# Optimization experiments

Measured on AMD Instinct MI355X. Metric: run time of the kernel, lower is better.

## Reference

```python
import jax, jax.numpy as jnp
import numpy as np

H = 32
W = 32
HIDDEN = 64
NUM_CLASSES = 10
BATCH = 128


def setup_inputs() -> dict:
    key = jax.random.key(0)
    ks = jax.random.split(key, 5)
    D = 4 * HIDDEN * H * W  # number_of_output_dimensions()
    return {
        "x": jax.random.normal(ks[0], (BATCH, 1, H, W), jnp.float32),
        "w_in": jax.random.normal(ks[1], (HIDDEN, 1), jnp.float32) * 0.1,
        "b_in": jnp.zeros((HIDDEN,), jnp.float32),
        "w_state": jax.random.normal(ks[2], (HIDDEN, HIDDEN, 2), jnp.float32) * (1.0 / np.sqrt(2 * HIDDEN)),
        "b_state": jnp.zeros((HIDDEN,), jnp.float32),
        "w_fc": jax.random.normal(ks[3], (D, NUM_CLASSES), jnp.float32) * 0.01,
        "b_fc": jnp.zeros((NUM_CLASSES,), jnp.float32),
    }


def _skew(x):
    # x: [B,1,H,W] -> [B,1,H,W+H-1]; row r shifted right by r (diagonal skew)
    Ws = W + H - 1
    col = jnp.arange(Ws)[None, :] - jnp.arange(H)[:, None]  # [H,Ws]
    valid = ((col >= 0) & (col < W)).astype(x.dtype)
    colc = jnp.clip(col, 0, W - 1)
    rows = jnp.arange(H)[:, None]
    return x[:, :, rows, colc] * valid[None, None]


def _one_direction(x, w_in, b_in, w_state, b_state):
    # Diagonal-scan MDRNN over skewed columns.
    B = x.shape[0]
    xs = _skew(x)  # [B,1,H,Ws]
    # Input projection for all columns at once (1x1 conv equivalent)
    xin = jnp.einsum('oc,bchw->bohw', w_in, xs) + b_in[None, :, None, None]
    cols = jnp.moveaxis(xin, 3, 0)  # [Ws,B,HIDDEN,H]

    w_up, w_same = w_state[:, :, 0], w_state[:, :, 1]

    def step(h, xc):
        # conv1d(kernel=2, padding=1) over column, bottom padding removed:
        # out[r] = w_up @ h[r-1] + w_same @ h[r]
        h_up = jnp.pad(h, ((0, 0), (0, 0), (1, 0)))[:, :, :H]
        s = (jnp.einsum('oi,bir->bor', w_up, h_up)
             + jnp.einsum('oi,bir->bor', w_same, h)
             + b_state[None, :, None])
        hn = jnp.tanh(s + xc)
        return hn, hn

    h0 = jnp.zeros((B, HIDDEN, H), x.dtype)
    _, ys = jax.lax.scan(step, h0, cols)  # [Ws,B,HIDDEN,H]
    acts = jnp.moveaxis(ys, 0, 3)  # [B,HIDDEN,H,Ws]
    # Unskew: out[..., r, c] = acts[..., r, c + r]
    ccols = jnp.arange(W)[None, :] + jnp.arange(H)[:, None]  # [H,W]
    rows = jnp.arange(H)[:, None]
    return acts[:, :, rows, ccols]  # [B,HIDDEN,H,W]


def reference(x, w_in, b_in, w_state, b_state, w_fc, b_fc):
    B = x.shape[0]
    # Four scanning directions via flips on dims 2 and 3, concatenated on batch
    x2 = x[:, :, ::-1, :]
    x3 = x[:, :, :, ::-1]
    x4 = x[:, :, ::-1, ::-1]
    xm = jnp.concatenate([x, x2, x3, x4], axis=0)  # [4B,1,H,W]
    acts = _one_direction(xm, w_in, b_in, w_state, b_state)  # [4B,HIDDEN,H,W]
    # index_select interleaving: example b gets its 4 direction copies contiguously
    sel = (jnp.arange(B)[:, None] + B * jnp.arange(4)[None, :]).reshape(-1)
    a = acts[sel].reshape(B, -1)  # [B, 4*HIDDEN*H*W]
    logits = a @ w_fc + b_fc
    return jax.nn.log_softmax(logits, axis=-1)
```

## Files before the change

kernel.cpp:

```cpp
#include <hip/hip_runtime.h>
#include <hip/hip_bf16.h>

#define NHID 64
#define NT   63
#define NBD  512
#define HLDS_STR 72
#define XSTR 35

typedef __attribute__((ext_vector_type(8))) short bf16x8;
typedef __attribute__((ext_vector_type(4))) float f32x4;

__device__ __forceinline__ float tanh_fast(float x) {
    const float e = __expf(2.0f * x);
    const float r = __builtin_amdgcn_rcpf(e + 1.0f);
    return 1.0f - 2.0f * r;
}

__device__ __forceinline__ unsigned int cvt_pk_bf16(float lo, float hi) {
    unsigned int r;
    asm("v_cvt_pk_bf16_f32 %0, %1, %2" : "=v"(r) : "v"(lo), "v"(hi));
    return r;
}

__device__ __forceinline__ float bf2f(unsigned int u16) {
    return __uint_as_float(u16 << 16);
}

#define SKEW_R0(t)  ((t) > 31 ? (t) - 31 : 0)
#define SKEW_R1(t)  ((t) < 31 ? (t) : 31)
#define SKEW_OFF(t) ((t) < 32 ? ((t) * ((t) + 1)) >> 1 : 1024 - (((63 - (t)) * (64 - (t))) >> 1))

#define LGKM_BARRIER() do {                                   \
    asm volatile("s_waitcnt lgkmcnt(0)" ::: "memory");        \
    __builtin_amdgcn_s_barrier();                             \
    asm volatile("" ::: "memory");                            \
} while (0)

__global__ __launch_bounds__(256, 4) void k_main(
    const float* __restrict__ x,
    const float* __restrict__ w_in,
    const float* __restrict__ b_in,
    const float* __restrict__ w_state,
    const float* __restrict__ b_state,
    unsigned short* __restrict__ acts_c,
    const float* __restrict__ w_fc,
    unsigned short* __restrict__ wt_swz)
{
    __shared__ __align__(16) unsigned short h0buf[33 * HLDS_STR];
    __shared__ __align__(16) unsigned short h1buf[33 * HLDS_STR];
    __shared__ float xs[32 * XSTR];

    const int tid = threadIdx.x;

    if (blockIdx.x >= 512) {
        const int rel = blockIdx.x - 512;
        const int t   = rel >> 6;
        const int sub = rel & 63;
        const int r0 = SKEW_R0(t), r1 = SKEW_R1(t);
        const int cnt = r1 - r0 + 1;
        const int span = cnt << 10;
        int f = sub * 2048 + tid * 8;
        const int fdst = f;
        if (f >= 4 * span) return;
        int d = 0;
        while (f >= span) { f -= span; ++d; }
        const int ks   = f >> 9;
        const int lane = (f >> 3) & 63;
        const int g = lane >> 4, n = lane & 15;
        unsigned int pk[4];
        #pragma unroll
        for (int jj = 0; jj < 4; ++jj) {
            float v[2] = {0.0f, 0.0f};
            #pragma unroll
            for (int h = 0; h < 2; ++h) {
                const int j = jj * 2 + h;
                const int k = ks * 32 + g * 8 + j;
                const int r = r0 + (k >> 6);
                const int o = k & 63;
                const int c = t - r;
                if (n < 10)
                    v[h] = w_fc[((((size_t)(d * 64 + o)) << 10) + (r << 5) + c) * 10 + n];
            }
            pk[jj] = cvt_pk_bf16(v[0], v[1]);
        }
        uint4 st; st.x = pk[0]; st.y = pk[1]; st.z = pk[2]; st.w = pk[3];
        *(uint4*)(wt_swz + (size_t)SKEW_OFF(t) * 4096 + fdst) = st;
        return;
    }

    const int bd  = blockIdx.x;
    const int d   = bd >> 7;
    const int b   = bd & 127;
    const int lane = tid & 63;
    const int wave = tid >> 6;
    const int wp = wave & 1;
    const int nt = wave >> 1;
    const int n  = lane & 15;
    const int g  = lane >> 4;

    const bool flr = (d & 1) != 0;
    const bool flc = (d & 2) != 0;
    const float* xb = x + (size_t)b * 1024;
    for (int idx = tid; idx < 1024; idx += 256) {
        const int r = idx >> 5, c = idx & 31;
        xs[r * XSTR + c] = xb[(flr ? 31 - r : r) * 32 + (flc ? 31 - c : c)];
    }

    for (int m2 = tid; m2 < (33 * HLDS_STR) / 2; m2 += 256) {
        ((unsigned int*)h0buf)[m2] = 0u;
        ((unsigned int*)h1buf)[m2] = 0u;
    }

    bf16x8 a0[4], a1[4];
    #pragma unroll
    for (int wl = 0; wl < 2; ++wl) {
        const int o = wp * 32 + wl * 16 + n;
        #pragma unroll
        for (int kt = 0; kt < 4; ++kt) {
            const int s  = kt >> 1;
            const int cb = (kt & 1) * 32 + g * 8;
            bf16x8 w8;
            #pragma unroll
            for (int j = 0; j < 8; ++j) {
                const float w = w_state[((size_t)o * 64 + cb + j) * 2 + s];
                w8[j] = (short)(cvt_pk_bf16(w, 0.0f) & 0xffffu);
            }
            if (wl == 0) a0[kt] = w8; else a1[kt] = w8;
        }
    }

    float biasr[2][4], winr[2][4];
    #pragma unroll
    for (int wl = 0; wl < 2; ++wl)
        #pragma unroll
        for (int j = 0; j < 4; ++j) {
            const int o = wp * 32 + wl * 16 + g * 4 + j;
            biasr[wl][j] = b_in[o] + b_state[o];
            winr[wl][j]  = w_in[o];
        }

    const int r_out = nt * 16 + n;
    const int rdoff = r_out * HLDS_STR + g * 8;
    const int wroff = (r_out + 1) * HLDS_STR;
    const int cb0 = wp * 32 + g * 4;
    const int tlo = nt * 16;
    const float* xs_r = &xs[r_out * XSTR];

    unsigned short* actp = acts_c + (size_t)bd * 65536 + (size_t)r_out * 1984 + cb0;

    __syncthreads();

#define STEP(T, RB, WB) do {                                                    \
    if ((unsigned)((T) - tlo) < 48u) {                                          \
        const bf16x8 b0 = *(const bf16x8*)&RB[rdoff];                           \
        const bf16x8 b1 = *(const bf16x8*)&RB[rdoff + 32];                      \
        const bf16x8 b2 = *(const bf16x8*)&RB[rdoff + HLDS_STR];                \
        const bf16x8 b3 = *(const bf16x8*)&RB[rdoff + HLDS_STR + 32];           \
        f32x4 s0a = {0,0,0,0}, s0b = {0,0,0,0};                                 \
        f32x4 s1a = {0,0,0,0}, s1b = {0,0,0,0};                                 \
        s0a = __builtin_amdgcn_mfma_f32_16x16x32_bf16(a0[0], b0, s0a, 0,0,0);   \
        s1a = __builtin_amdgcn_mfma_f32_16x16x32_bf16(a1[0], b0, s1a, 0,0,0);   \
        s0b = __builtin_amdgcn_mfma_f32_16x16x32_bf16(a0[2], b2, s0b, 0,0,0);   \
        s1b = __builtin_amdgcn_mfma_f32_16x16x32_bf16(a1[2], b2, s1b, 0,0,0);   \
        s0a = __builtin_amdgcn_mfma_f32_16x16x32_bf16(a0[1], b1, s0a, 0,0,0);   \
        s1a = __builtin_amdgcn_mfma_f32_16x16x32_bf16(a1[1], b1, s1a, 0,0,0);   \
        s0b = __builtin_amdgcn_mfma_f32_16x16x32_bf16(a0[3], b3, s0b, 0,0,0);   \
        s1b = __builtin_amdgcn_mfma_f32_16x16x32_bf16(a1[3], b3, s1b, 0,0,0);   \
        const int c_ = (T) - r_out;                                             \
        const float xv = ((unsigned)c_ < 32u) ? xs_r[c_ & 31] : 0.0f;           \
        uint2 pk0, pk1;                                                         \
        {                                                                       \
            const float h0 = tanh_fast(s0a[0] + s0b[0] + biasr[0][0] + winr[0][0] * xv); \
            const float h1 = tanh_fast(s0a[1] + s0b[1] + biasr[0][1] + winr[0][1] * xv); \
            const float h2 = tanh_fast(s0a[2] + s0b[2] + biasr[0][2] + winr[0][2] * xv); \
            const float h3 = tanh_fast(s0a[3] + s0b[3] + biasr[0][3] + winr[0][3] * xv); \
            pk0.x = cvt_pk_bf16(h0, h1); pk0.y = cvt_pk_bf16(h2, h3);           \
            *(uint2*)&WB[wroff + cb0] = pk0;                                    \
        }                                                                       \
        {                                                                       \
            const float h0 = tanh_fast(s1a[0] + s1b[0] + biasr[1][0] + winr[1][0] * xv); \
            const float h1 = tanh_fast(s1a[1] + s1b[1] + biasr[1][1] + winr[1][1] * xv); \
            const float h2 = tanh_fast(s1a[2] + s1b[2] + biasr[1][2] + winr[1][2] * xv); \
            const float h3 = tanh_fast(s1a[3] + s1b[3] + biasr[1][3] + winr[1][3] * xv); \
            pk1.x = cvt_pk_bf16(h0, h1); pk1.y = cvt_pk_bf16(h2, h3);           \
            *(uint2*)&WB[wroff + cb0 + 16] = pk1;                               \
        }                                                                       \
        if ((unsigned)c_ < 32u) {                                               \
            *(uint2*)(actp)      = pk0;                                         \
            *(uint2*)(actp + 16) = pk1;                                         \
        }                                                                       \
    }                                                                           \
    LGKM_BARRIER();                                                             \
    actp += 64;                                                                 \
} while (0)

    for (int sp = 0; sp < 31; ++sp) {
        const int t = 2 * sp;
        STEP(t,     h0buf, h1buf);
        STEP(t + 1, h1buf, h0buf);
    }
    STEP(62, h0buf, h1buf);
#undef STEP
}

__global__ __launch_bounds__(256, 4) void k_fc(
    const unsigned short* __restrict__ acts_c,
    const unsigned short* __restrict__ wt_swz,
    float* __restrict__ partial)
{
    const int tid = threadIdx.x;
    const int blk = blockIdx.x;
    const int t   = blk >> 3;
    const int d   = (blk >> 1) & 3;
    const int mh  = blk & 1;
    const int lane = tid & 63;
    const int wv  = tid >> 6;
    const int g   = lane >> 4;
    const int n   = lane & 15;

    const int r0 = SKEW_R0(t), r1 = SKEW_R1(t);
    const int cnt = r1 - r0 + 1;
    const int off = SKEW_OFF(t);

    const int tb = d * 128 + mh * 64 + wv * 16;
    const unsigned short* Ap = acts_c + (size_t)(tb + n) * 65536
                             + (size_t)r0 * 1984 + (size_t)t * 64 + g * 8;
    const unsigned short* Bp = wt_swz
        + ((size_t)off * 4 + (size_t)d * cnt) * 1024 + lane * 8;

    f32x4 acc = {0.f, 0.f, 0.f, 0.f};
    #pragma unroll 2
    for (int q = 0; q < cnt; ++q) {
        const bf16x8 a0  = *(const bf16x8*)(Ap);
        const bf16x8 bb0 = *(const bf16x8*)(Bp);
        const bf16x8 a1  = *(const bf16x8*)(Ap + 32);
        const bf16x8 bb1 = *(const bf16x8*)(Bp + 512);
        acc = __builtin_amdgcn_mfma_f32_16x16x32_bf16(a0, bb0, acc, 0, 0, 0);
        acc = __builtin_amdgcn_mfma_f32_16x16x32_bf16(a1, bb1, acc, 0, 0, 0);
        Ap += 1984;
        Bp += 1024;
    }
    const int batch = tb + g * 4;
    #pragma unroll
    for (int reg = 0; reg < 4; ++reg)
        partial[((size_t)t * 512 + batch + reg) * 16 + n] = acc[reg];
}

__global__ __launch_bounds__(256) void k_out(
    const float* __restrict__ partial,
    const float* __restrict__ b_fc,
    float* __restrict__ out)
{
    __shared__ float lred[252 * 10];
    __shared__ float lgs[10];
    __shared__ float lse;
    const int b = blockIdx.x;
    const int tid = threadIdx.x;
    if (tid < 252) {
        const int t = tid >> 2, d = tid & 3;
        const float* p = partial + ((size_t)t * 512 + d * 128 + b) * 16;
        #pragma unroll
        for (int n2 = 0; n2 < 10; ++n2) lred[tid * 10 + n2] = p[n2];
    }
    __syncthreads();
    if (tid < 10) {
        float s = b_fc[tid];
        for (int i = 0; i < 252; ++i) s += lred[i * 10 + tid];
        lgs[tid] = s;
    }
    __syncthreads();
    if (tid == 0) {
        float m = lgs[0];
        for (int nn = 1; nn < 10; ++nn) m = fmaxf(m, lgs[nn]);
        float ssum = 0.0f;
        for (int nn = 0; nn < 10; ++nn) ssum += __expf(lgs[nn] - m);
        lse = m + __logf(ssum);
    }
    __syncthreads();
    if (tid < 10) out[b * 10 + tid] = lgs[tid] - lse;
}

extern "C" void kernel_launch(void* const* d_in, const int* in_sizes, int n_in,
                              void* d_out, int out_size, void* d_ws, size_t ws_size,
                              hipStream_t stream)
{
    const float* x       = (const float*)d_in[0];
    const float* w_in    = (const float*)d_in[1];
    const float* b_in    = (const float*)d_in[2];
    const float* w_state = (const float*)d_in[3];
    const float* b_state = (const float*)d_in[4];
    const float* w_fc    = (const float*)d_in[5];
    const float* b_fc    = (const float*)d_in[6];
    float* out = (float*)d_out;

    unsigned short* wt_swz = (unsigned short*)d_ws;
    float* partial = (float*)((char*)d_ws + (size_t)(8u << 20));
    unsigned short* acts_c = (unsigned short*)((char*)d_ws + (size_t)(16u << 20));

    k_main<<<4544, 256, 0, stream>>>(x, w_in, b_in, w_state, b_state,
                                     acts_c, w_fc, wt_swz);
    k_fc  <<<504, 256, 0, stream>>>(acts_c, wt_swz, partial);
    k_out <<<128, 256, 0, stream>>>(partial, b_fc, out);
}
```

Baseline: 62.83 us.

## Replace block barriers with inter-wave LDS flags using two-wave recurrence blocks

The recurrence blocks shrink from four waves to two. Each wave now owns 16 rows and computes all 64 hidden outputs with 16 MFMAs per step. The per-step workgroup barrier is replaced by point-to-point LDS flags, where each wave spins with s_sleep until the partner wave has finished the previous step. The weight-prep blocks now process two chunks per thread to match the smaller block size. This aims to cut barrier cost, but doubles the serial MFMA and epilogue work per wave each step and adds spin-wait latency.

```diff
diff --git a/kernel.cpp b/kernel.cpp
--- a/kernel.cpp
+++ b/kernel.cpp
@@ -30,13 +30,38 @@
 #define SKEW_R1(t)  ((t) < 31 ? (t) : 31)
 #define SKEW_OFF(t) ((t) < 32 ? ((t) * ((t) + 1)) >> 1 : 1024 - (((63 - (t)) * (64 - (t))) >> 1))
 
-#define LGKM_BARRIER() do {                                   \
-    asm volatile("s_waitcnt lgkmcnt(0)" ::: "memory");        \
-    __builtin_amdgcn_s_barrier();                             \
-    asm volatile("" ::: "memory");                            \
-} while (0)
-
-__global__ __launch_bounds__(256, 4) void k_main(
+__device__ __forceinline__ void prep_one(
+    const float* __restrict__ w_fc, unsigned short* __restrict__ wt_swz,
+    int t, int r0, int span, int f)
+{
+    if (f >= 4 * span) return;
+    const int fdst = f;
+    int d = 0;
+    while (f >= span) { f -= span; ++d; }
+    const int ks   = f >> 9;
+    const int lane = (f >> 3) & 63;
+    const int g = lane >> 4, n = lane & 15;
+    unsigned int pk[4];
+    #pragma unroll
+    for (int jj = 0; jj < 4; ++jj) {
+        float v[2] = {0.0f, 0.0f};
+        #pragma unroll
+        for (int h = 0; h < 2; ++h) {
+            const int j = jj * 2 + h;
+            const int k = ks * 32 + g * 8 + j;
+            const int r = r0 + (k >> 6);
+            const int o = k & 63;
+            const int c = t - r;
+            if (n < 10)
+                v[h] = w_fc[((((size_t)(d * 64 + o)) << 10) + (r << 5) + c) * 10 + n];
+        }
+        pk[jj] = cvt_pk_bf16(v[0], v[1]);
+    }
+    uint4 st; st.x = pk[0]; st.y = pk[1]; st.z = pk[2]; st.w = pk[3];
+    *(uint4*)(wt_swz + (size_t)SKEW_OFF(t) * 4096 + fdst) = st;
+}
+
+__global__ __launch_bounds__(128, 2) void k_main(
     const float* __restrict__ x,
     const float* __restrict__ w_in,
     const float* __restrict__ b_in,
@@ -49,6 +74,7 @@
     __shared__ __align__(16) unsigned short h0buf[33 * HLDS_STR];
     __shared__ __align__(16) unsigned short h1buf[33 * HLDS_STR];
     __shared__ float xs[32 * XSTR];
+    __shared__ int sflags[2];
 
     const int tid = threadIdx.x;
 
@@ -57,34 +83,10 @@
         const int t   = rel >> 6;
         const int sub = rel & 63;
         const int r0 = SKEW_R0(t), r1 = SKEW_R1(t);
-        const int cnt = r1 - r0 + 1;
-        const int span = cnt << 10;
-        int f = sub * 2048 + tid * 8;
-        const int fdst = f;
-        if (f >= 4 * span) return;
-        int d = 0;
-        while (f >= span) { f -= span; ++d; }
-        const int ks   = f >> 9;
-        const int lane = (f >> 3) & 63;
-        const int g = lane >> 4, n = lane & 15;
-        unsigned int pk[4];
-        #pragma unroll
-        for (int jj = 0; jj < 4; ++jj) {
-            float v[2] = {0.0f, 0.0f};
-            #pragma unroll
-            for (int h = 0; h < 2; ++h) {
-                const int j = jj * 2 + h;
-                const int k = ks * 32 + g * 8 + j;
-                const int r = r0 + (k >> 6);
-                const int o = k & 63;
-                const int c = t - r;
-                if (n < 10)
-                    v[h] = w_fc[((((size_t)(d * 64 + o)) << 10) + (r << 5) + c) * 10 + n];
-            }
-            pk[jj] = cvt_pk_bf16(v[0], v[1]);
-        }
-        uint4 st; st.x = pk[0]; st.y = pk[1]; st.z = pk[2]; st.w = pk[3];
-        *(uint4*)(wt_swz + (size_t)SKEW_OFF(t) * 4096 + fdst) = st;
+        const int span = (r1 - r0 + 1) << 10;
+        const int f1 = sub * 2048 + tid * 8;
+        prep_one(w_fc, wt_swz, t, r0, span, f1);
+        prep_one(w_fc, wt_swz, t, r0, span, f1 + 1024);
         return;
     }
 
@@ -93,28 +95,27 @@
     const int b   = bd & 127;
     const int lane = tid & 63;
     const int wave = tid >> 6;
-    const int wp = wave & 1;
-    const int nt = wave >> 1;
     const int n  = lane & 15;
     const int g  = lane >> 4;
 
     const bool flr = (d & 1) != 0;
     const bool flc = (d & 2) != 0;
     const float* xb = x + (size_t)b * 1024;
-    for (int idx = tid; idx < 1024; idx += 256) {
+    for (int idx = tid; idx < 1024; idx += 128) {
         const int r = idx >> 5, c = idx & 31;
         xs[r * XSTR + c] = xb[(flr ? 31 - r : r) * 32 + (flc ? 31 - c : c)];
     }
 
-    for (int m2 = tid; m2 < (33 * HLDS_STR) / 2; m2 += 256) {
+    for (int m2 = tid; m2 < (33 * HLDS_STR) / 2; m2 += 128) {
         ((unsigned int*)h0buf)[m2] = 0u;
         ((unsigned int*)h1buf)[m2] = 0u;
     }
-
-    bf16x8 a0[4], a1[4];
+    if (tid == 0) { sflags[0] = 0; sflags[1] = 0; }
+
+    bf16x8 a[4][4];
     #pragma unroll
-    for (int wl = 0; wl < 2; ++wl) {
-        const int o = wp * 32 + wl * 16 + n;
+    for (int mt = 0; mt < 4; ++mt) {
+        const int o = mt * 16 + n;
         #pragma unroll
         for (int kt = 0; kt < 4; ++kt) {
             const int s  = kt >> 1;
@@ -125,73 +126,69 @@
                 const float w = w_state[((size_t)o * 64 + cb + j) * 2 + s];
                 w8[j] = (short)(cvt_pk_bf16(w, 0.0f) & 0xffffu);
             }
-            if (wl == 0) a0[kt] = w8; else a1[kt] = w8;
+            a[mt][kt] = w8;
         }
     }
 
-    float biasr[2][4], winr[2][4];
+    float biasr[4][4], winr[4][4];
     #pragma unroll
-    for (int wl = 0; wl < 2; ++wl)
+    for (int mt = 0; mt < 4; ++mt)
         #pragma unroll
         for (int j = 0; j < 4; ++j) {
-            const int o = wp * 32 + wl * 16 + g * 4 + j;
-            biasr[wl][j] = b_in[o] + b_state[o];
-            winr[wl][j]  = w_in[o];
+            const int o = mt * 16 + g * 4 + j;
+            biasr[mt][j] = b_in[o] + b_state[o];
+            winr[mt][j]  = w_in[o];
         }
 
-    const int r_out = nt * 16 + n;
+    const int r_out = wave * 16 + n;
     const int rdoff = r_out * HLDS_STR + g * 8;
-    const int wroff = (r_out + 1) * HLDS_STR;
-    const int cb0 = wp * 32 + g * 4;
-    const int tlo = nt * 16;
+    const int wroff = (r_out + 1) * HLDS_STR + g * 4;
+    const int tlo = wave * 16;
     const float* xs_r = &xs[r_out * XSTR];
-
-    unsigned short* actp = acts_c + (size_t)bd * 65536 + (size_t)r_out * 1984 + cb0;
+    volatile int* my_flag = (volatile int*)&sflags[wave];
+    volatile int* ot_flag = (volatile int*)&sflags[wave ^ 1];
+
+    unsigned short* actp = acts_c + (size_t)bd * 65536 + (size_t)r_out * 1984 + g * 4;
 
     __syncthreads();
 
-#define STEP(T, RB, WB) do {                                                    \
-    if ((unsigned)((T) - tlo) < 48u) {                                          \
-        const bf16x8 b0 = *(const bf16x8*)&RB[rdoff];                           \
-        const bf16x8 b1 = *(const bf16x8*)&RB[rdoff + 32];                      \
-        const bf16x8 b2 = *(const bf16x8*)&RB[rdoff + HLDS_STR];                \
-        const bf16x8 b3 = *(const bf16x8*)&RB[rdoff + HLDS_STR + 32];           \
-        f32x4 s0a = {0,0,0,0}, s0b = {0,0,0,0};                                 \
-        f32x4 s1a = {0,0,0,0}, s1b = {0,0,0,0};                                 \
-        s0a = __builtin_amdgcn_mfma_f32_16x16x32_bf16(a0[0], b0, s0a, 0,0,0);   \
-        s1a = __builtin_amdgcn_mfma_f32_16x16x32_bf16(a1[0], b0, s1a, 0,0,0);   \
-        s0b = __builtin_amdgcn_mfma_f32_16x16x32_bf16(a0[2], b2, s0b, 0,0,0);   \
-        s1b = __builtin_amdgcn_mfma_f32_16x16x32_bf16(a1[2], b2, s1b, 0,0,0);   \
-        s0a = __builtin_amdgcn_mfma_f32_16x16x32_bf16(a0[1], b1, s0a, 0,0,0);   \
-        s1a = __builtin_amdgcn_mfma_f32_16x16x32_bf16(a1[1], b1, s1a, 0,0,0);   \
-        s0b = __builtin_amdgcn_mfma_f32_16x16x32_bf16(a0[3], b3, s0b, 0,0,0);   \
-        s1b = __builtin_amdgcn_mfma_f32_16x16x32_bf16(a1[3], b3, s1b, 0,0,0);   \
-        const int c_ = (T) - r_out;                                             \
-        const float xv = ((unsigned)c_ < 32u) ? xs_r[c_ & 31] : 0.0f;           \
-        uint2 pk0, pk1;                                                         \
-        {                                                                       \
-            const float h0 = tanh_fast(s0a[0] + s0b[0] + biasr[0][0] + winr[0][0] * xv); \
-            const float h1 = tanh_fast(s0a[1] + s0b[1] + biasr[0][1] + winr[0][1] * xv); \
-            const float h2 = tanh_fast(s0a[2] + s0b[2] + biasr[0][2] + winr[0][2] * xv); \
-            const float h3 = tanh_fast(s0a[3] + s0b[3] + biasr[0][3] + winr[0][3] * xv); \
-            pk0.x = cvt_pk_bf16(h0, h1); pk0.y = cvt_pk_bf16(h2, h3);           \
-            *(uint2*)&WB[wroff + cb0] = pk0;                                    \
-        }                                                                       \
-        {                                                                       \
-            const float h0 = tanh_fast(s1a[0] + s1b[0] + biasr[1][0] + winr[1][0] * xv); \
-            const float h1 = tanh_fast(s1a[1] + s1b[1] + biasr[1][1] + winr[1][1] * xv); \
-            const float h2 = tanh_fast(s1a[2] + s1b[2] + biasr[1][2] + winr[1][2] * xv); \
-            const float h3 = tanh_fast(s1a[3] + s1b[3] + biasr[1][3] + winr[1][3] * xv); \
-            pk1.x = cvt_pk_bf16(h0, h1); pk1.y = cvt_pk_bf16(h2, h3);           \
-            *(uint2*)&WB[wroff + cb0 + 16] = pk1;                               \
-        }                                                                       \
-        if ((unsigned)c_ < 32u) {                                               \
-            *(uint2*)(actp)      = pk0;                                         \
-            *(uint2*)(actp + 16) = pk1;                                         \
-        }                                                                       \
-    }                                                                           \
-    LGKM_BARRIER();                                                             \
-    actp += 64;                                                                 \
+#define MFMA(F, B, C) C = __builtin_amdgcn_mfma_f32_16x16x32_bf16(F, B, C, 0, 0, 0)
+#define EPI(MT, AA, BB, WBUF) {                                                  \
+    const float h0 = tanh_fast(AA[0] + BB[0] + biasr[MT][0] + winr[MT][0] * xv); \
+    const float h1 = tanh_fast(AA[1] + BB[1] + biasr[MT][1] + winr[MT][1] * xv); \
+    const float h2 = tanh_fast(AA[2] + BB[2] + biasr[MT][2] + winr[MT][2] * xv); \
+    const float h3 = tanh_fast(AA[3] + BB[3] + biasr[MT][3] + winr[MT][3] * xv); \
+    uint2 pk; pk.x = cvt_pk_bf16(h0, h1); pk.y = cvt_pk_bf16(h2, h3);            \
+    *(uint2*)&WBUF[wroff + (MT) * 16] = pk;                                      \
+    if (stv) *(uint2*)(actp + (MT) * 16) = pk;                                   \
+}
+
+#define STEP(T, RB, WB) do {                                                     \
+    if ((unsigned)((T) - tlo) < 48u) {                                           \
+        while (*ot_flag < (T)) __builtin_amdgcn_s_sleep(1);                      \
+        const bf16x8 b0 = *(const bf16x8*)&RB[rdoff];                            \
+        const bf16x8 b1 = *(const bf16x8*)&RB[rdoff + 32];                       \
+        const bf16x8 b2 = *(const bf16x8*)&RB[rdoff + HLDS_STR];                 \
+        const bf16x8 b3 = *(const bf16x8*)&RB[rdoff + HLDS_STR + 32];            \
+        f32x4 A0 = {0,0,0,0}, A1 = {0,0,0,0}, A2 = {0,0,0,0}, A3 = {0,0,0,0};    \
+        f32x4 B0 = {0,0,0,0}, B1 = {0,0,0,0}, B2 = {0,0,0,0}, B3 = {0,0,0,0};    \
+        MFMA(a[0][0], b0, A0); MFMA(a[1][0], b0, A1);                            \
+        MFMA(a[2][0], b0, A2); MFMA(a[3][0], b0, A3);                            \
+        MFMA(a[0][2], b2, B0); MFMA(a[1][2], b2, B1);                            \
+        MFMA(a[2][2], b2, B2); MFMA(a[3][2], b2, B3);                            \
+        MFMA(a[0][1], b1, A0); MFMA(a[1][1], b1, A1);                            \
+        MFMA(a[2][1], b1, A2); MFMA(a[3][1], b1, A3);                            \
+        MFMA(a[0][3], b3, B0); MFMA(a[1][3], b3, B1);                            \
+        MFMA(a[2][3], b3, B2); MFMA(a[3][3], b3, B3);                            \
+        const int c_ = (T) - r_out;                                              \
+        const bool stv = (unsigned)c_ < 32u;                                     \
+        const float xv = stv ? xs_r[c_ & 31] : 0.0f;                             \
+        EPI(0, A0, B0, WB); EPI(1, A1, B1, WB);                                  \
+        EPI(2, A2, B2, WB); EPI(3, A3, B3, WB);                                  \
+        asm volatile("s_waitcnt lgkmcnt(0)" ::: "memory");                       \
+    }                                                                            \
+    if (lane == 0) *my_flag = (T) + 1;                                           \
+    actp += 64;                                                                  \
 } while (0)
 
     for (int sp = 0; sp < 31; ++sp) {
@@ -201,6 +198,8 @@
     }
     STEP(62, h0buf, h1buf);
 #undef STEP
+#undef EPI
+#undef MFMA
 }
 
 __global__ __launch_bounds__(256, 4) void k_fc(
@@ -297,7 +296,7 @@
     float* partial = (float*)((char*)d_ws + (size_t)(8u << 20));
     unsigned short* acts_c = (unsigned short*)((char*)d_ws + (size_t)(16u << 20));
 
-    k_main<<<4544, 256, 0, stream>>>(x, w_in, b_in, w_state, b_state,
+    k_main<<<4544, 128, 0, stream>>>(x, w_in, b_in, w_state, b_state,
                                      acts_c, w_fc, wt_swz);
     k_fc  <<<504, 256, 0, stream>>>(acts_c, wt_swz, partial);
     k_out <<<128, 256, 0, stream>>>(partial, b_fc, out);
```

Result: slower. 95.86 us (+52.6%).

## Process two batch sequences per block in recurrent scan kernel

Applied to the files above, without the earlier changes.

Each recurrent block now carries two independent (direction, batch) sequences through the diagonal scan, so the MFMA state-weight fragments are reused and the per-step barrier is shared by two sequences. This halves the number of scan blocks and doubles the independent MFMA work between barriers, which should hide latency in the serial 63-step chain. The cost is twice the shared memory per block, more registers, and a launch bound lowered to 2 blocks per SM. Total parallelism also drops to 256 scan blocks.

```diff
diff --git a/kernel.cpp b/kernel.cpp
--- a/kernel.cpp
+++ b/kernel.cpp
@@ -36,7 +36,7 @@
     asm volatile("" ::: "memory");                            \
 } while (0)
 
-__global__ __launch_bounds__(256, 4) void k_main(
+__global__ __launch_bounds__(256, 2) void k_main(
     const float* __restrict__ x,
     const float* __restrict__ w_in,
     const float* __restrict__ b_in,
@@ -46,14 +46,17 @@
     const float* __restrict__ w_fc,
     unsigned short* __restrict__ wt_swz)
 {
-    __shared__ __align__(16) unsigned short h0buf[33 * HLDS_STR];
-    __shared__ __align__(16) unsigned short h1buf[33 * HLDS_STR];
-    __shared__ float xs[32 * XSTR];
+    __shared__ __align__(16) unsigned short hA0[33 * HLDS_STR];
+    __shared__ __align__(16) unsigned short hA1[33 * HLDS_STR];
+    __shared__ __align__(16) unsigned short hB0[33 * HLDS_STR];
+    __shared__ __align__(16) unsigned short hB1[33 * HLDS_STR];
+    __shared__ float xsA[32 * XSTR];
+    __shared__ float xsB[32 * XSTR];
 
     const int tid = threadIdx.x;
 
-    if (blockIdx.x >= 512) {
-        const int rel = blockIdx.x - 512;
+    if (blockIdx.x >= 256) {
+        const int rel = blockIdx.x - 256;
         const int t   = rel >> 6;
         const int sub = rel & 63;
         const int r0 = SKEW_R0(t), r1 = SKEW_R1(t);
@@ -88,9 +91,11 @@
         return;
     }
 
-    const int bd  = blockIdx.x;
-    const int d   = bd >> 7;
-    const int b   = bd & 127;
+    const int blk = blockIdx.x;
+    const int bdA = 2 * blk;
+    const int bdB = 2 * blk + 1;
+    const int d   = bdA >> 7;
+    const int bA  = bdA & 127;
     const int lane = tid & 63;
     const int wave = tid >> 6;
     const int wp = wave & 1;
@@ -100,15 +105,19 @@
 
     const bool flr = (d & 1) != 0;
     const bool flc = (d & 2) != 0;
-    const float* xb = x + (size_t)b * 1024;
+    const float* xbA = x + (size_t)bA * 1024;
     for (int idx = tid; idx < 1024; idx += 256) {
         const int r = idx >> 5, c = idx & 31;
-        xs[r * XSTR + c] = xb[(flr ? 31 - r : r) * 32 + (flc ? 31 - c : c)];
+        const int src = (flr ? 31 - r : r) * 32 + (flc ? 31 - c : c);
+        xsA[r * XSTR + c] = xbA[src];
+        xsB[r * XSTR + c] = xbA[1024 + src];
     }
 
     for (int m2 = tid; m2 < (33 * HLDS_STR) / 2; m2 += 256) {
-        ((unsigned int*)h0buf)[m2] = 0u;
-        ((unsigned int*)h1buf)[m2] = 0u;
+        ((unsigned int*)hA0)[m2] = 0u;
+        ((unsigned int*)hA1)[m2] = 0u;
+        ((unsigned int*)hB0)[m2] = 0u;
+        ((unsigned int*)hB1)[m2] = 0u;
     }
 
     bf16x8 a0[4], a1[4];
@@ -144,63 +153,67 @@
     const int wroff = (r_out + 1) * HLDS_STR;
     const int cb0 = wp * 32 + g * 4;
     const int tlo = nt * 16;
-    const float* xs_r = &xs[r_out * XSTR];
-
-    unsigned short* actp = acts_c + (size_t)bd * 65536 + (size_t)r_out * 1984 + cb0;
+    const float* xsA_r = &xsA[r_out * XSTR];
+    const float* xsB_r = &xsB[r_out * XSTR];
+
+    unsigned short* actpA = acts_c + (size_t)bdA * 65536 + (size_t)r_out * 1984 + cb0;
+    unsigned short* actpB = acts_c + (size_t)bdB * 65536 + (size_t)r_out * 1984 + cb0;
 
     __syncthreads();
 
-#define STEP(T, RB, WB) do {                                                    \
-    if ((unsigned)((T) - tlo) < 48u) {                                          \
-        const bf16x8 b0 = *(const bf16x8*)&RB[rdoff];                           \
-        const bf16x8 b1 = *(const bf16x8*)&RB[rdoff + 32];                      \
-        const bf16x8 b2 = *(const bf16x8*)&RB[rdoff + HLDS_STR];                \
-        const bf16x8 b3 = *(const bf16x8*)&RB[rdoff + HLDS_STR + 32];           \
-        f32x4 s0a = {0,0,0,0}, s0b = {0,0,0,0};                                 \
-        f32x4 s1a = {0,0,0,0}, s1b = {0,0,0,0};                                 \
-        s0a = __builtin_amdgcn_mfma_f32_16x16x32_bf16(a0[0], b0, s0a, 0,0,0);   \
-        s1a = __builtin_amdgcn_mfma_f32_16x16x32_bf16(a1[0], b0, s1a, 0,0,0);   \
-        s0b = __builtin_amdgcn_mfma_f32_16x16x32_bf16(a0[2], b2, s0b, 0,0,0);   \
-        s1b = __builtin_amdgcn_mfma_f32_16x16x32_bf16(a1[2], b2, s1b, 0,0,0);   \
-        s0a = __builtin_amdgcn_mfma_f32_16x16x32_bf16(a0[1], b1, s0a, 0,0,0);   \
-        s1a = __builtin_amdgcn_mfma_f32_16x16x32_bf16(a1[1], b1, s1a, 0,0,0);   \
-        s0b = __builtin_amdgcn_mfma_f32_16x16x32_bf16(a0[3], b3, s0b, 0,0,0);   \
-        s1b = __builtin_amdgcn_mfma_f32_16x16x32_bf16(a1[3], b3, s1b, 0,0,0);   \
-        const int c_ = (T) - r_out;                                             \
-        const float xv = ((unsigned)c_ < 32u) ? xs_r[c_ & 31] : 0.0f;           \
-        uint2 pk0, pk1;                                                         \
-        {                                                                       \
-            const float h0 = tanh_fast(s0a[0] + s0b[0] + biasr[0][0] + winr[0][0] * xv); \
-            const float h1 = tanh_fast(s0a[1] + s0b[1] + biasr[0][1] + winr[0][1] * xv); \
-            const float h2 = tanh_fast(s0a[2] + s0b[2] + biasr[0][2] + winr[0][2] * xv); \
-            const float h3 = tanh_fast(s0a[3] + s0b[3] + biasr[0][3] + winr[0][3] * xv); \
-            pk0.x = cvt_pk_bf16(h0, h1); pk0.y = cvt_pk_bf16(h2, h3);           \
-            *(uint2*)&WB[wroff + cb0] = pk0;                                    \
-        }                                                                       \
-        {                                                                       \
-            const float h0 = tanh_fast(s1a[0] + s1b[0] + biasr[1][0] + winr[1][0] * xv); \
-            const float h1 = tanh_fast(s1a[1] + s1b[1] + biasr[1][1] + winr[1][1] * xv); \
-            const float h2 = tanh_fast(s1a[2] + s1b[2] + biasr[1][2] + winr[1][2] * xv); \
-            const float h3 = tanh_fast(s1a[3] + s1b[3] + biasr[1][3] + winr[1][3] * xv); \
-            pk1.x = cvt_pk_bf16(h0, h1); pk1.y = cvt_pk_bf16(h2, h3);           \
-            *(uint2*)&WB[wroff + cb0 + 16] = pk1;                               \
-        }                                                                       \
-        if ((unsigned)c_ < 32u) {                                               \
-            *(uint2*)(actp)      = pk0;                                         \
-            *(uint2*)(actp + 16) = pk1;                                         \
-        }                                                                       \
-    }                                                                           \
-    LGKM_BARRIER();                                                             \
-    actp += 64;                                                                 \
+#define MFMA(F, B, C) C = __builtin_amdgcn_mfma_f32_16x16x32_bf16(F, B, C, 0, 0, 0)
+#define EPI(WL, SA, SB, XV, WBUF, ACTP) {                                        \
+    const float h0 = tanh_fast(SA[0] + SB[0] + biasr[WL][0] + winr[WL][0] * (XV)); \
+    const float h1 = tanh_fast(SA[1] + SB[1] + biasr[WL][1] + winr[WL][1] * (XV)); \
+    const float h2 = tanh_fast(SA[2] + SB[2] + biasr[WL][2] + winr[WL][2] * (XV)); \
+    const float h3 = tanh_fast(SA[3] + SB[3] + biasr[WL][3] + winr[WL][3] * (XV)); \
+    uint2 pk; pk.x = cvt_pk_bf16(h0, h1); pk.y = cvt_pk_bf16(h2, h3);            \
+    *(uint2*)&WBUF[wroff + cb0 + (WL) * 16] = pk;                                \
+    if (stv) *(uint2*)((ACTP) + (WL) * 16) = pk;                                 \
+}
+
+#define STEP(T, RA_, WA_, RB_, WB_) do {                                         \
+    if ((unsigned)((T) - tlo) < 48u) {                                           \
+        const bf16x8 fA0 = *(const bf16x8*)&RA_[rdoff];                          \
+        const bf16x8 fA1 = *(const bf16x8*)&RA_[rdoff + 32];                     \
+        const bf16x8 fA2 = *(const bf16x8*)&RA_[rdoff + HLDS_STR];               \
+        const bf16x8 fA3 = *(const bf16x8*)&RA_[rdoff + HLDS_STR + 32];          \
+        const bf16x8 fB0 = *(const bf16x8*)&RB_[rdoff];                          \
+        const bf16x8 fB1 = *(const bf16x8*)&RB_[rdoff + 32];                     \
+        const bf16x8 fB2 = *(const bf16x8*)&RB_[rdoff + HLDS_STR];               \
+        const bf16x8 fB3 = *(const bf16x8*)&RB_[rdoff + HLDS_STR + 32];          \
+        f32x4 sA0a = {0,0,0,0}, sA0b = {0,0,0,0};                                \
+        f32x4 sA1a = {0,0,0,0}, sA1b = {0,0,0,0};                                \
+        f32x4 sB0a = {0,0,0,0}, sB0b = {0,0,0,0};                                \
+        f32x4 sB1a = {0,0,0,0}, sB1b = {0,0,0,0};                                \
+        MFMA(a0[0], fA0, sA0a); MFMA(a1[0], fA0, sA1a);                          \
+        MFMA(a0[0], fB0, sB0a); MFMA(a1[0], fB0, sB1a);                          \
+        MFMA(a0[2], fA2, sA0b); MFMA(a1[2], fA2, sA1b);                          \
+        MFMA(a0[2], fB2, sB0b); MFMA(a1[2], fB2, sB1b);                          \
+        MFMA(a0[1], fA1, sA0a); MFMA(a1[1], fA1, sA1a);                          \
+        MFMA(a0[1], fB1, sB0a); MFMA(a1[1], fB1, sB1a);                          \
+        MFMA(a0[3], fA3, sA0b); MFMA(a1[3], fA3, sA1b);                          \
+        MFMA(a0[3], fB3, sB0b); MFMA(a1[3], fB3, sB1b);                          \
+        const int c_ = (T) - r_out;                                              \
+        const bool stv = (unsigned)c_ < 32u;                                     \
+        const float xvA = stv ? xsA_r[c_ & 31] : 0.0f;                           \
+        const float xvB = stv ? xsB_r[c_ & 31] : 0.0f;                           \
+        EPI(0, sA0a, sA0b, xvA, WA_, actpA); EPI(1, sA1a, sA1b, xvA, WA_, actpA);\
+        EPI(0, sB0a, sB0b, xvB, WB_, actpB); EPI(1, sB1a, sB1b, xvB, WB_, actpB);\
+    }                                                                            \
+    LGKM_BARRIER();                                                              \
+    actpA += 64; actpB += 64;                                                    \
 } while (0)
 
     for (int sp = 0; sp < 31; ++sp) {
         const int t = 2 * sp;
-        STEP(t,     h0buf, h1buf);
-        STEP(t + 1, h1buf, h0buf);
-    }
-    STEP(62, h0buf, h1buf);
+        STEP(t,     hA0, hA1, hB0, hB1);
+        STEP(t + 1, hA1, hA0, hB1, hB0);
+    }
+    STEP(62, hA0, hA1, hB0, hB1);
 #undef STEP
+#undef EPI
+#undef MFMA
 }
 
 __global__ __launch_bounds__(256, 4) void k_fc(
@@ -297,7 +310,7 @@
     float* partial = (float*)((char*)d_ws + (size_t)(8u << 20));
     unsigned short* acts_c = (unsigned short*)((char*)d_ws + (size_t)(16u << 20));
 
-    k_main<<<4544, 256, 0, stream>>>(x, w_in, b_in, w_state, b_state,
+    k_main<<<4288, 256, 0, stream>>>(x, w_in, b_in, w_state, b_state,
                                      acts_c, w_fc, wt_swz);
     k_fc  <<<504, 256, 0, stream>>>(acts_c, wt_swz, partial);
     k_out <<<128, 256, 0, stream>>>(partial, b_fc, out);
```

Result: slower. 76.93 us (+22.4%).
